# Optimization experiments

Hardware: AMD Instinct MI355X
Metric: run time of the kernel (lower is better)

Reference implementation:

```python
import jax, jax.numpy as jnp
import numpy as np

N = 4_194_304   # samples per polarization
L = 513         # impulse response taps


def setup_inputs() -> dict:
    key = jax.random.key(0)
    k1, k2, k3, k4 = jax.random.split(key, 4)
    tx_real = jax.random.normal(k1, (2, N), dtype=jnp.float32)
    tx_imag = jax.random.normal(k2, (2, N), dtype=jnp.float32)
    h_real = jax.random.normal(k3, (L,), dtype=jnp.float32)
    h_imag = jax.random.normal(k4, (L,), dtype=jnp.float32)
    return {"tx_real": tx_real, "tx_imag": tx_imag, "h_real": h_real, "h_imag": h_imag}


def reference(tx_real, tx_imag, h_real, h_imag):
    # Dual-pol complex baseband signal [2, N]; same taps h [L] applied to each pol.
    tx = tx_real + 1j * tx_imag          # complex64 [2, N]
    h = h_real + 1j * h_imag             # complex64 [L]
    n_out = tx.shape[-1] + h.shape[0] - 1  # 'full' convolution length
    # FFT-based full convolution, both polarizations batched in one FFT call
    # (mathematically identical to overlap-save convolution in 'full' mode).
    X = jnp.fft.fft(tx, n=n_out, axis=-1)   # [2, n_out]
    H = jnp.fft.fft(h, n=n_out)             # [n_out]
    y = jnp.fft.ifft(X * H[None, :], axis=-1)  # [2, n_out] complex
    # Return real/imag stacked so the output is a real array: [2, n_out, 2]
    return jnp.stack([y.real, y.imag], axis=-1)
```

## Files before the change

### kernel.cpp

```cpp
#include <hip/hip_runtime.h>
#include <hip/hip_bf16.h>


#define NSAMP 4194304
#define LTAPS 513
#define NOUT  (NSAMP + LTAPS - 1)

#define BLK       256
#define WAVES     4
#define WAVE_OUT  1024
#define BLOCK_OUT 4096
#define HALO      512
#define XELEMS    (BLOCK_OUT + HALO + 16)
#define NB        34
#define HROWS     568
#define NBLK      ((NOUT + BLOCK_OUT - 1) / BLOCK_OUT)

typedef __attribute__((ext_vector_type(8)))  short short8;
typedef __attribute__((ext_vector_type(4)))  short short4v;
typedef __attribute__((ext_vector_type(16))) float float16v;

__device__ __forceinline__ int xswz(int e) { return e + ((e >> 5) << 3); }
#define XSZ 5776

__device__ __forceinline__ short f2b(float f) {
    __bf16 b = (__bf16)f;
    return __builtin_bit_cast(short, b);
}

__global__ __launch_bounds__(BLK)
void build_h(const float* __restrict__ hr, const float* __restrict__ hi,
             short* __restrict__ hh) {
    int R = blockIdx.x * BLK + threadIdx.x;
    if (R < HROWS) {
        short8 vr, vi, vn;
        #pragma unroll
        for (int j = 0; j < 8; ++j) {
            int idx = R - 24 - j;
            bool ok = (idx >= 0) && (idx < LTAPS);
            float fr = ok ? hr[idx] : 0.0f;
            float fi = ok ? hi[idx] : 0.0f;
            vr[j] = f2b(fr);
            vi[j] = f2b(fi);
            vn[j] = f2b(-fi);
        }
        *(short8*)(hh + (size_t)(0 * HROWS + R) * 8) = vr;
        *(short8*)(hh + (size_t)(1 * HROWS + R) * 8) = vi;
        *(short8*)(hh + (size_t)(2 * HROWS + R) * 8) = vn;
    }
}

__global__ __launch_bounds__(BLK, 4)
void fir_mfma32(const float* __restrict__ txr_all, const float* __restrict__ txi_all,
                const short* __restrict__ hh, float2* __restrict__ out) {
    const int pol = blockIdx.y;
    const int N0  = blockIdx.x * BLOCK_OUT;
    const int tid = threadIdx.x;

    __shared__ short xr_s[XSZ];
    __shared__ short xi_s[XSZ];

    const float* __restrict__ xr_g = txr_all + (size_t)pol * NSAMP;
    const float* __restrict__ xi_g = txi_all + (size_t)pol * NSAMP;

    #pragma unroll
    for (int it = 0; it < 5; ++it) {
        int e = (tid + it * BLK) * 4;
        if (e < XELEMS) {
            int g = N0 - HALO + e;
            float r0, r1, r2, r3, i0, i1, i2, i3;
            if (g >= 0 && g + 3 < NSAMP) {
                float4 fr = *(const float4*)(xr_g + g);
                float4 fi = *(const float4*)(xi_g + g);
                r0 = fr.x; r1 = fr.y; r2 = fr.z; r3 = fr.w;
                i0 = fi.x; i1 = fi.y; i2 = fi.z; i3 = fi.w;
            } else {
                int gc0 = min(max(g + 0, 0), NSAMP - 1);
                int gc1 = min(max(g + 1, 0), NSAMP - 1);
                int gc2 = min(max(g + 2, 0), NSAMP - 1);
                int gc3 = min(max(g + 3, 0), NSAMP - 1);
                r0 = (g + 0 >= 0 && g + 0 < NSAMP) ? xr_g[gc0] : 0.0f;
                r1 = (g + 1 >= 0 && g + 1 < NSAMP) ? xr_g[gc1] : 0.0f;
                r2 = (g + 2 >= 0 && g + 2 < NSAMP) ? xr_g[gc2] : 0.0f;
                r3 = (g + 3 >= 0 && g + 3 < NSAMP) ? xr_g[gc3] : 0.0f;
                i0 = (g + 0 >= 0 && g + 0 < NSAMP) ? xi_g[gc0] : 0.0f;
                i1 = (g + 1 >= 0 && g + 1 < NSAMP) ? xi_g[gc1] : 0.0f;
                i2 = (g + 2 >= 0 && g + 2 < NSAMP) ? xi_g[gc2] : 0.0f;
                i3 = (g + 3 >= 0 && g + 3 < NSAMP) ? xi_g[gc3] : 0.0f;
            }
            int ls = xswz(e);
            short4v vr = { f2b(r0), f2b(r1), f2b(r2), f2b(r3) };
            short4v vi = { f2b(i0), f2b(i1), f2b(i2), f2b(i3) };
            *(short4v*)(xr_s + ls) = vr;
            *(short4v*)(xi_s + ls) = vi;
        }
    }
    __syncthreads();

    const int lane = tid & 63;
    const int wave = tid >> 6;
    const int cc   = lane & 31;
    const int half = lane >> 5;

    float16v acc_re = {0.f,0.f,0.f,0.f,0.f,0.f,0.f,0.f,0.f,0.f,0.f,0.f,0.f,0.f,0.f,0.f};
    float16v acc_im = {0.f,0.f,0.f,0.f,0.f,0.f,0.f,0.f,0.f,0.f,0.f,0.f,0.f,0.f,0.f,0.f};

    const int   ebase = HALO + wave * WAVE_OUT + 32 * cc + 8 * half + 16;
    const short* hp0  = hh + (size_t)(cc - 8 * half + 8) * 8;

    for (int b = 0; b < NB; ++b) {
        const short* hp = hp0 + (size_t)(16 * b) * 8;
        short8 fhr = *(const short8*)(hp);
        short8 fhi = *(const short8*)(hp + (size_t)HROWS * 8);
        short8 fnh = *(const short8*)(hp + (size_t)(2 * HROWS) * 8);
        int ls = xswz(ebase - 16 * b);
        short8 fxr = *(const short8*)(xr_s + ls);
        short8 fxi = *(const short8*)(xi_s + ls);
        acc_re = __builtin_amdgcn_mfma_f32_32x32x16_bf16(fxr, fhr, acc_re, 0, 0, 0);
        acc_re = __builtin_amdgcn_mfma_f32_32x32x16_bf16(fxi, fnh, acc_re, 0, 0, 0);
        acc_im = __builtin_amdgcn_mfma_f32_32x32x16_bf16(fxr, fhi, acc_im, 0, 0, 0);
        acc_im = __builtin_amdgcn_mfma_f32_32x32x16_bf16(fxi, fhr, acc_im, 0, 0, 0);
    }

    float2* __restrict__ op = out + (size_t)pol * NOUT;
    const int nw = N0 + wave * WAVE_OUT;
    #pragma unroll
    for (int v = 0; v < 16; ++v) {
        int row = (v & 3) + 8 * (v >> 2) + 4 * half;
        int n = nw + 32 * row + cc;
        if (n < NOUT) op[n] = make_float2(acc_re[v], acc_im[v]);
    }
}

extern "C" void kernel_launch(void* const* d_in, const int* in_sizes, int n_in,
                              void* d_out, int out_size, void* d_ws, size_t ws_size,
                              hipStream_t stream) {
    const float* txr = (const float*)d_in[0];
    const float* txi = (const float*)d_in[1];
    const float* hr  = (const float*)d_in[2];
    const float* hi  = (const float*)d_in[3];
    float2* out = (float2*)d_out;
    short* hh = (short*)d_ws;

    build_h<<<dim3((HROWS + BLK - 1) / BLK), BLK, 0, stream>>>(hr, hi, hh);

    dim3 grid(NBLK, 2);
    fir_mfma32<<<grid, BLK, 0, stream>>>(txr, txi, hh, out);
}
```

Baseline: 147.2 us.

## Process both polarizations per block and software-pipeline MFMA operand loads

Each block now stages both polarizations in shared memory and computes both with the same filter fragments, so each tap fragment loaded from global/L2 feeds twice as many MFMAs and the grid shrinks by half. The tap loop prefetches the next iteration's filter and signal fragments before issuing the current MFMAs, which overlaps load latency with matrix math. The cost is doubled LDS per block and more accumulator registers, so occupancy drops (launch bound lowered to 3) and there are fewer blocks to spread across CUs.

```diff
diff --git a/kernel.cpp b/kernel.cpp
--- a/kernel.cpp
+++ b/kernel.cpp
@@ -7,7 +7,6 @@
 #define NOUT  (NSAMP + LTAPS - 1)
 
 #define BLK       256
-#define WAVES     4
 #define WAVE_OUT  1024
 #define BLOCK_OUT 4096
 #define HALO      512
@@ -50,49 +49,52 @@
     }
 }
 
-__global__ __launch_bounds__(BLK, 4)
-void fir_mfma32(const float* __restrict__ txr_all, const float* __restrict__ txi_all,
-                const short* __restrict__ hh, float2* __restrict__ out) {
-    const int pol = blockIdx.y;
+#define MFMA32(A, B, C) __builtin_amdgcn_mfma_f32_32x32x16_bf16((A), (B), (C), 0, 0, 0)
+
+__global__ __launch_bounds__(BLK, 3)
+void fir_mfma32dp(const float* __restrict__ txr_all, const float* __restrict__ txi_all,
+                  const short* __restrict__ hh, float2* __restrict__ out) {
     const int N0  = blockIdx.x * BLOCK_OUT;
     const int tid = threadIdx.x;
 
-    __shared__ short xr_s[XSZ];
-    __shared__ short xi_s[XSZ];
-
-    const float* __restrict__ xr_g = txr_all + (size_t)pol * NSAMP;
-    const float* __restrict__ xi_g = txi_all + (size_t)pol * NSAMP;
+    __shared__ short xr_s[2][XSZ];
+    __shared__ short xi_s[2][XSZ];
 
     #pragma unroll
-    for (int it = 0; it < 5; ++it) {
-        int e = (tid + it * BLK) * 4;
-        if (e < XELEMS) {
-            int g = N0 - HALO + e;
-            float r0, r1, r2, r3, i0, i1, i2, i3;
-            if (g >= 0 && g + 3 < NSAMP) {
-                float4 fr = *(const float4*)(xr_g + g);
-                float4 fi = *(const float4*)(xi_g + g);
-                r0 = fr.x; r1 = fr.y; r2 = fr.z; r3 = fr.w;
-                i0 = fi.x; i1 = fi.y; i2 = fi.z; i3 = fi.w;
-            } else {
-                int gc0 = min(max(g + 0, 0), NSAMP - 1);
-                int gc1 = min(max(g + 1, 0), NSAMP - 1);
-                int gc2 = min(max(g + 2, 0), NSAMP - 1);
-                int gc3 = min(max(g + 3, 0), NSAMP - 1);
-                r0 = (g + 0 >= 0 && g + 0 < NSAMP) ? xr_g[gc0] : 0.0f;
-                r1 = (g + 1 >= 0 && g + 1 < NSAMP) ? xr_g[gc1] : 0.0f;
-                r2 = (g + 2 >= 0 && g + 2 < NSAMP) ? xr_g[gc2] : 0.0f;
-                r3 = (g + 3 >= 0 && g + 3 < NSAMP) ? xr_g[gc3] : 0.0f;
-                i0 = (g + 0 >= 0 && g + 0 < NSAMP) ? xi_g[gc0] : 0.0f;
-                i1 = (g + 1 >= 0 && g + 1 < NSAMP) ? xi_g[gc1] : 0.0f;
-                i2 = (g + 2 >= 0 && g + 2 < NSAMP) ? xi_g[gc2] : 0.0f;
-                i3 = (g + 3 >= 0 && g + 3 < NSAMP) ? xi_g[gc3] : 0.0f;
+    for (int p = 0; p < 2; ++p) {
+        const float* __restrict__ xr_g = txr_all + (size_t)p * NSAMP;
+        const float* __restrict__ xi_g = txi_all + (size_t)p * NSAMP;
+        #pragma unroll
+        for (int it = 0; it < 5; ++it) {
+            int e = (tid + it * BLK) * 4;
+            if (e < XELEMS) {
+                int g = N0 - HALO + e;
+                float r0, r1, r2, r3, i0, i1, i2, i3;
+                if (g >= 0 && g + 3 < NSAMP) {
+                    float4 fr = *(const float4*)(xr_g + g);
+                    float4 fi = *(const float4*)(xi_g + g);
+                    r0 = fr.x; r1 = fr.y; r2 = fr.z; r3 = fr.w;
+                    i0 = fi.x; i1 = fi.y; i2 = fi.z; i3 = fi.w;
+                } else {
+                    int gc0 = min(max(g + 0, 0), NSAMP - 1);
+                    int gc1 = min(max(g + 1, 0), NSAMP - 1);
+                    int gc2 = min(max(g + 2, 0), NSAMP - 1);
+                    int gc3 = min(max(g + 3, 0), NSAMP - 1);
+                    r0 = (g + 0 >= 0 && g + 0 < NSAMP) ? xr_g[gc0] : 0.0f;
+                    r1 = (g + 1 >= 0 && g + 1 < NSAMP) ? xr_g[gc1] : 0.0f;
+                    r2 = (g + 2 >= 0 && g + 2 < NSAMP) ? xr_g[gc2] : 0.0f;
+                    r3 = (g + 3 >= 0 && g + 3 < NSAMP) ? xr_g[gc3] : 0.0f;
+                    i0 = (g + 0 >= 0 && g + 0 < NSAMP) ? xi_g[gc0] : 0.0f;
+                    i1 = (g + 1 >= 0 && g + 1 < NSAMP) ? xi_g[gc1] : 0.0f;
+                    i2 = (g + 2 >= 0 && g + 2 < NSAMP) ? xi_g[gc2] : 0.0f;
+                    i3 = (g + 3 >= 0 && g + 3 < NSAMP) ? xi_g[gc3] : 0.0f;
+                }
+                int ls = xswz(e);
+                short4v vr = { f2b(r0), f2b(r1), f2b(r2), f2b(r3) };
+                short4v vi = { f2b(i0), f2b(i1), f2b(i2), f2b(i3) };
+                *(short4v*)(&xr_s[p][ls]) = vr;
+                *(short4v*)(&xi_s[p][ls]) = vi;
             }
-            int ls = xswz(e);
-            short4v vr = { f2b(r0), f2b(r1), f2b(r2), f2b(r3) };
-            short4v vi = { f2b(i0), f2b(i1), f2b(i2), f2b(i3) };
-            *(short4v*)(xr_s + ls) = vr;
-            *(short4v*)(xi_s + ls) = vi;
         }
     }
     __syncthreads();
@@ -102,33 +104,59 @@
     const int cc   = lane & 31;
     const int half = lane >> 5;
 
-    float16v acc_re = {0.f,0.f,0.f,0.f,0.f,0.f,0.f,0.f,0.f,0.f,0.f,0.f,0.f,0.f,0.f,0.f};
-    float16v acc_im = {0.f,0.f,0.f,0.f,0.f,0.f,0.f,0.f,0.f,0.f,0.f,0.f,0.f,0.f,0.f,0.f};
+    float16v accr0 = {0.f,0.f,0.f,0.f,0.f,0.f,0.f,0.f,0.f,0.f,0.f,0.f,0.f,0.f,0.f,0.f};
+    float16v acci0 = accr0, accr1 = accr0, acci1 = accr0;
 
-    const int   ebase = HALO + wave * WAVE_OUT + 32 * cc + 8 * half + 16;
-    const short* hp0  = hh + (size_t)(cc - 8 * half + 8) * 8;
+    const int    ebase = HALO + wave * WAVE_OUT + 32 * cc + 8 * half + 16;
+    const short* hp0   = hh + (size_t)(cc - 8 * half + 8) * 8;
 
+    short8 fhr  = *(const short8*)(hp0);
+    short8 fhi  = *(const short8*)(hp0 + (size_t)HROWS * 8);
+    short8 fnh  = *(const short8*)(hp0 + (size_t)(2 * HROWS) * 8);
+    int ls0 = xswz(ebase);
+    short8 fxr0 = *(const short8*)(&xr_s[0][ls0]);
+    short8 fxi0 = *(const short8*)(&xi_s[0][ls0]);
+    short8 fxr1 = *(const short8*)(&xr_s[1][ls0]);
+    short8 fxi1 = *(const short8*)(&xi_s[1][ls0]);
+
+    #pragma unroll 2
     for (int b = 0; b < NB; ++b) {
-        const short* hp = hp0 + (size_t)(16 * b) * 8;
-        short8 fhr = *(const short8*)(hp);
-        short8 fhi = *(const short8*)(hp + (size_t)HROWS * 8);
-        short8 fnh = *(const short8*)(hp + (size_t)(2 * HROWS) * 8);
-        int ls = xswz(ebase - 16 * b);
-        short8 fxr = *(const short8*)(xr_s + ls);
-        short8 fxi = *(const short8*)(xi_s + ls);
-        acc_re = __builtin_amdgcn_mfma_f32_32x32x16_bf16(fxr, fhr, acc_re, 0, 0, 0);
-        acc_re = __builtin_amdgcn_mfma_f32_32x32x16_bf16(fxi, fnh, acc_re, 0, 0, 0);
-        acc_im = __builtin_amdgcn_mfma_f32_32x32x16_bf16(fxr, fhi, acc_im, 0, 0, 0);
-        acc_im = __builtin_amdgcn_mfma_f32_32x32x16_bf16(fxi, fhr, acc_im, 0, 0, 0);
+        int bn = (b + 1 < NB) ? (b + 1) : 0;
+        const short* hpn = hp0 + (size_t)(16 * bn) * 8;
+        short8 nhr = *(const short8*)(hpn);
+        short8 nhi = *(const short8*)(hpn + (size_t)HROWS * 8);
+        short8 nnh = *(const short8*)(hpn + (size_t)(2 * HROWS) * 8);
+        int lsn = xswz(ebase - 16 * bn);
+        short8 nxr0 = *(const short8*)(&xr_s[0][lsn]);
+        short8 nxi0 = *(const short8*)(&xi_s[0][lsn]);
+        short8 nxr1 = *(const short8*)(&xr_s[1][lsn]);
+        short8 nxi1 = *(const short8*)(&xi_s[1][lsn]);
+
+        accr0 = MFMA32(fxr0, fhr, accr0);
+        accr0 = MFMA32(fxi0, fnh, accr0);
+        acci0 = MFMA32(fxr0, fhi, acci0);
+        acci0 = MFMA32(fxi0, fhr, acci0);
+        accr1 = MFMA32(fxr1, fhr, accr1);
+        accr1 = MFMA32(fxi1, fnh, accr1);
+        acci1 = MFMA32(fxr1, fhi, acci1);
+        acci1 = MFMA32(fxi1, fhr, acci1);
+
+        fhr = nhr; fhi = nhi; fnh = nnh;
+        fxr0 = nxr0; fxi0 = nxi0; fxr1 = nxr1; fxi1 = nxi1;
     }
 
-    float2* __restrict__ op = out + (size_t)pol * NOUT;
     const int nw = N0 + wave * WAVE_OUT;
     #pragma unroll
-    for (int v = 0; v < 16; ++v) {
-        int row = (v & 3) + 8 * (v >> 2) + 4 * half;
-        int n = nw + 32 * row + cc;
-        if (n < NOUT) op[n] = make_float2(acc_re[v], acc_im[v]);
+    for (int p = 0; p < 2; ++p) {
+        float2* __restrict__ op = out + (size_t)p * NOUT;
+        const float16v& ar = p ? accr1 : accr0;
+        const float16v& ai = p ? acci1 : acci0;
+        #pragma unroll
+        for (int v = 0; v < 16; ++v) {
+            int row = (v & 3) + 8 * (v >> 2) + 4 * half;
+            int n = nw + 32 * row + cc;
+            if (n < NOUT) op[n] = make_float2(ar[v], ai[v]);
+        }
     }
 }
 
@@ -144,6 +172,5 @@
 
     build_h<<<dim3((HROWS + BLK - 1) / BLK), BLK, 0, stream>>>(hr, hi, hh);
 
-    dim3 grid(NBLK, 2);
-    fir_mfma32<<<grid, BLK, 0, stream>>>(txr, txi, hh, out);
+    fir_mfma32dp<<<dim3(NBLK), BLK, 0, stream>>>(txr, txi, hh, out);
 }
```

Result: no change. 146.5 us (-0.4%).

## Process both polarizations per block and negate imag input with sign-bit XOR

Applied to the files above, without the earlier changes.

Each block now loads both polarizations for a 2048-sample output strip. Two waves handle each polarization, so the grid is no longer split over polarization. The separate negated-h table is dropped and the negation is applied to the x imaginary fragment with an XOR on the bf16 sign bits, which cuts one global/L2 load of h per iteration. The smaller block raises the halo overhead ratio, since the 512-sample halo is now loaded relative to 2048 outputs per polarization instead of 4096, and the launch-bounds occupancy hint moves from 4 to 5.

```diff
diff --git a/kernel.cpp b/kernel.cpp
--- a/kernel.cpp
+++ b/kernel.cpp
@@ -7,9 +7,8 @@
 #define NOUT  (NSAMP + LTAPS - 1)
 
 #define BLK       256
-#define WAVES     4
 #define WAVE_OUT  1024
-#define BLOCK_OUT 4096
+#define BLOCK_OUT 2048
 #define HALO      512
 #define XELEMS    (BLOCK_OUT + HALO + 16)
 #define NB        34
@@ -18,10 +17,11 @@
 
 typedef __attribute__((ext_vector_type(8)))  short short8;
 typedef __attribute__((ext_vector_type(4)))  short short4v;
+typedef __attribute__((ext_vector_type(4)))  int   int4v;
 typedef __attribute__((ext_vector_type(16))) float float16v;
 
 __device__ __forceinline__ int xswz(int e) { return e + ((e >> 5) << 3); }
-#define XSZ 5776
+#define XSZ 3224
 
 __device__ __forceinline__ short f2b(float f) {
     __bf16 b = (__bf16)f;
@@ -33,97 +33,106 @@
              short* __restrict__ hh) {
     int R = blockIdx.x * BLK + threadIdx.x;
     if (R < HROWS) {
-        short8 vr, vi, vn;
+        short8 vr, vi;
         #pragma unroll
         for (int j = 0; j < 8; ++j) {
             int idx = R - 24 - j;
             bool ok = (idx >= 0) && (idx < LTAPS);
-            float fr = ok ? hr[idx] : 0.0f;
-            float fi = ok ? hi[idx] : 0.0f;
-            vr[j] = f2b(fr);
-            vi[j] = f2b(fi);
-            vn[j] = f2b(-fi);
+            vr[j] = f2b(ok ? hr[idx] : 0.0f);
+            vi[j] = f2b(ok ? hi[idx] : 0.0f);
         }
         *(short8*)(hh + (size_t)(0 * HROWS + R) * 8) = vr;
         *(short8*)(hh + (size_t)(1 * HROWS + R) * 8) = vi;
-        *(short8*)(hh + (size_t)(2 * HROWS + R) * 8) = vn;
     }
 }
 
-__global__ __launch_bounds__(BLK, 4)
-void fir_mfma32(const float* __restrict__ txr_all, const float* __restrict__ txi_all,
-                const short* __restrict__ hh, float2* __restrict__ out) {
-    const int pol = blockIdx.y;
+#define MFMA32(A, B, C) __builtin_amdgcn_mfma_f32_32x32x16_bf16((A), (B), (C), 0, 0, 0)
+
+__device__ __forceinline__ short8 bneg8(short8 v) {
+    int4v t = __builtin_bit_cast(int4v, v);
+    t ^= (int4v){(int)0x80008000, (int)0x80008000, (int)0x80008000, (int)0x80008000};
+    return __builtin_bit_cast(short8, t);
+}
+
+__global__ __launch_bounds__(BLK, 5)
+void fir_mfma32w(const float* __restrict__ txr_all, const float* __restrict__ txi_all,
+                 const short* __restrict__ hh, float2* __restrict__ out) {
     const int N0  = blockIdx.x * BLOCK_OUT;
     const int tid = threadIdx.x;
 
-    __shared__ short xr_s[XSZ];
-    __shared__ short xi_s[XSZ];
-
-    const float* __restrict__ xr_g = txr_all + (size_t)pol * NSAMP;
-    const float* __restrict__ xi_g = txi_all + (size_t)pol * NSAMP;
+    __shared__ __align__(16) short xr_s[2][XSZ];
+    __shared__ __align__(16) short xi_s[2][XSZ];
 
     #pragma unroll
-    for (int it = 0; it < 5; ++it) {
-        int e = (tid + it * BLK) * 4;
-        if (e < XELEMS) {
-            int g = N0 - HALO + e;
-            float r0, r1, r2, r3, i0, i1, i2, i3;
-            if (g >= 0 && g + 3 < NSAMP) {
-                float4 fr = *(const float4*)(xr_g + g);
-                float4 fi = *(const float4*)(xi_g + g);
-                r0 = fr.x; r1 = fr.y; r2 = fr.z; r3 = fr.w;
-                i0 = fi.x; i1 = fi.y; i2 = fi.z; i3 = fi.w;
-            } else {
-                int gc0 = min(max(g + 0, 0), NSAMP - 1);
-                int gc1 = min(max(g + 1, 0), NSAMP - 1);
-                int gc2 = min(max(g + 2, 0), NSAMP - 1);
-                int gc3 = min(max(g + 3, 0), NSAMP - 1);
-                r0 = (g + 0 >= 0 && g + 0 < NSAMP) ? xr_g[gc0] : 0.0f;
-                r1 = (g + 1 >= 0 && g + 1 < NSAMP) ? xr_g[gc1] : 0.0f;
-                r2 = (g + 2 >= 0 && g + 2 < NSAMP) ? xr_g[gc2] : 0.0f;
-                r3 = (g + 3 >= 0 && g + 3 < NSAMP) ? xr_g[gc3] : 0.0f;
-                i0 = (g + 0 >= 0 && g + 0 < NSAMP) ? xi_g[gc0] : 0.0f;
-                i1 = (g + 1 >= 0 && g + 1 < NSAMP) ? xi_g[gc1] : 0.0f;
-                i2 = (g + 2 >= 0 && g + 2 < NSAMP) ? xi_g[gc2] : 0.0f;
-                i3 = (g + 3 >= 0 && g + 3 < NSAMP) ? xi_g[gc3] : 0.0f;
+    for (int p = 0; p < 2; ++p) {
+        const float* __restrict__ xr_g = txr_all + (size_t)p * NSAMP;
+        const float* __restrict__ xi_g = txi_all + (size_t)p * NSAMP;
+        #pragma unroll
+        for (int it = 0; it < 3; ++it) {
+            int e = (tid + it * BLK) * 4;
+            if (e < XELEMS) {
+                int g = N0 - HALO + e;
+                float r0, r1, r2, r3, i0, i1, i2, i3;
+                if (g >= 0 && g + 3 < NSAMP) {
+                    float4 fr = *(const float4*)(xr_g + g);
+                    float4 fi = *(const float4*)(xi_g + g);
+                    r0 = fr.x; r1 = fr.y; r2 = fr.z; r3 = fr.w;
+                    i0 = fi.x; i1 = fi.y; i2 = fi.z; i3 = fi.w;
+                } else {
+                    int gc0 = min(max(g + 0, 0), NSAMP - 1);
+                    int gc1 = min(max(g + 1, 0), NSAMP - 1);
+                    int gc2 = min(max(g + 2, 0), NSAMP - 1);
+                    int gc3 = min(max(g + 3, 0), NSAMP - 1);
+                    r0 = (g + 0 >= 0 && g + 0 < NSAMP) ? xr_g[gc0] : 0.0f;
+                    r1 = (g + 1 >= 0 && g + 1 < NSAMP) ? xr_g[gc1] : 0.0f;
+                    r2 = (g + 2 >= 0 && g + 2 < NSAMP) ? xr_g[gc2] : 0.0f;
+                    r3 = (g + 3 >= 0 && g + 3 < NSAMP) ? xr_g[gc3] : 0.0f;
+                    i0 = (g + 0 >= 0 && g + 0 < NSAMP) ? xi_g[gc0] : 0.0f;
+                    i1 = (g + 1 >= 0 && g + 1 < NSAMP) ? xi_g[gc1] : 0.0f;
+                    i2 = (g + 2 >= 0 && g + 2 < NSAMP) ? xi_g[gc2] : 0.0f;
+                    i3 = (g + 3 >= 0 && g + 3 < NSAMP) ? xi_g[gc3] : 0.0f;
+                }
+                int ls = xswz(e);
+                short4v vr = { f2b(r0), f2b(r1), f2b(r2), f2b(r3) };
+                short4v vi = { f2b(i0), f2b(i1), f2b(i2), f2b(i3) };
+                *(short4v*)(&xr_s[p][ls]) = vr;
+                *(short4v*)(&xi_s[p][ls]) = vi;
             }
-            int ls = xswz(e);
-            short4v vr = { f2b(r0), f2b(r1), f2b(r2), f2b(r3) };
-            short4v vi = { f2b(i0), f2b(i1), f2b(i2), f2b(i3) };
-            *(short4v*)(xr_s + ls) = vr;
-            *(short4v*)(xi_s + ls) = vi;
         }
     }
     __syncthreads();
 
     const int lane = tid & 63;
     const int wave = tid >> 6;
+    const int pol  = wave >> 1;
+    const int strip = wave & 1;
     const int cc   = lane & 31;
     const int half = lane >> 5;
 
     float16v acc_re = {0.f,0.f,0.f,0.f,0.f,0.f,0.f,0.f,0.f,0.f,0.f,0.f,0.f,0.f,0.f,0.f};
-    float16v acc_im = {0.f,0.f,0.f,0.f,0.f,0.f,0.f,0.f,0.f,0.f,0.f,0.f,0.f,0.f,0.f,0.f};
+    float16v acc_im = acc_re;
 
-    const int   ebase = HALO + wave * WAVE_OUT + 32 * cc + 8 * half + 16;
-    const short* hp0  = hh + (size_t)(cc - 8 * half + 8) * 8;
+    const int    ebase = HALO + strip * WAVE_OUT + 32 * cc + 8 * half + 16;
+    const short* hp0   = hh + (size_t)(cc - 8 * half + 8) * 8;
+    const short* xrp   = xr_s[pol];
+    const short* xip   = xi_s[pol];
 
     for (int b = 0; b < NB; ++b) {
         const short* hp = hp0 + (size_t)(16 * b) * 8;
         short8 fhr = *(const short8*)(hp);
         short8 fhi = *(const short8*)(hp + (size_t)HROWS * 8);
-        short8 fnh = *(const short8*)(hp + (size_t)(2 * HROWS) * 8);
         int ls = xswz(ebase - 16 * b);
-        short8 fxr = *(const short8*)(xr_s + ls);
-        short8 fxi = *(const short8*)(xi_s + ls);
-        acc_re = __builtin_amdgcn_mfma_f32_32x32x16_bf16(fxr, fhr, acc_re, 0, 0, 0);
-        acc_re = __builtin_amdgcn_mfma_f32_32x32x16_bf16(fxi, fnh, acc_re, 0, 0, 0);
-        acc_im = __builtin_amdgcn_mfma_f32_32x32x16_bf16(fxr, fhi, acc_im, 0, 0, 0);
-        acc_im = __builtin_amdgcn_mfma_f32_32x32x16_bf16(fxi, fhr, acc_im, 0, 0, 0);
+        short8 fxr = *(const short8*)(xrp + ls);
+        short8 fxi = *(const short8*)(xip + ls);
+        short8 fnxi = bneg8(fxi);
+        acc_re = MFMA32(fxr,  fhr, acc_re);
+        acc_re = MFMA32(fnxi, fhi, acc_re);
+        acc_im = MFMA32(fxi,  fhr, acc_im);
+        acc_im = MFMA32(fxr,  fhi, acc_im);
     }
 
     float2* __restrict__ op = out + (size_t)pol * NOUT;
-    const int nw = N0 + wave * WAVE_OUT;
+    const int nw = N0 + strip * WAVE_OUT;
     #pragma unroll
     for (int v = 0; v < 16; ++v) {
         int row = (v & 3) + 8 * (v >> 2) + 4 * half;
@@ -144,6 +153,5 @@
 
     build_h<<<dim3((HROWS + BLK - 1) / BLK), BLK, 0, stream>>>(hr, hi, hh);
 
-    dim3 grid(NBLK, 2);
-    fir_mfma32<<<grid, BLK, 0, stream>>>(txr, txi, hh, out);
+    fir_mfma32w<<<dim3(NBLK), BLK, 0, stream>>>(txr, txi, hh, out);
 }
```

After: 140.4 us. 1.05x faster.
